# Kernel tuning notes

Measured on AMD Instinct MI355X. Metric: run time of the kernel, lower is better.

## Reference

```python
import jax, jax.numpy as jnp
import numpy as np

# Static config (matches init_kwargs / chosen shapes)
B, H, W, C, NH, WS, SS = 8, 56, 56, 1024, 32, 7, 3
N = WS * WS            # tokens per window = 49
HID = 4 * C            # mlp hidden dim
HEAD = C // NH         # 32
SCALE = HEAD ** -0.5


def _rel_pos_index():
    # Same construction as the torch buffer `relative_position_index`
    coords = np.stack(np.meshgrid(np.arange(WS), np.arange(WS), indexing='ij'))  # (2, WS, WS)
    cf = coords.reshape(2, -1)                                    # (2, N)
    rel = (cf[:, :, None] - cf[:, None, :]).transpose(1, 2, 0)    # (N, N, 2)
    rel = rel.copy()
    rel[:, :, 0] += WS - 1
    rel[:, :, 1] += WS - 1
    rel[:, :, 0] *= 2 * WS - 1
    return jnp.asarray(rel.sum(-1))                               # (N, N) int

RPI = _rel_pos_index()


def _shift_mask():
    # Standard Swin cyclic-shift attention mask (0 / -100) for Hp=H, Wp=W
    img = np.zeros((1, H, W, 1), dtype=np.float32)
    cnt = 0
    for hs in (slice(0, -WS), slice(-WS, -SS), slice(-SS, None)):
        for ws in (slice(0, -WS), slice(-WS, -SS), slice(-SS, None)):
            img[:, hs, ws, :] = cnt
            cnt += 1
    mw = img.reshape(1, H // WS, WS, W // WS, WS, 1).transpose(0, 1, 3, 2, 4, 5).reshape(-1, N)
    diff = mw[:, None, :] - mw[:, :, None]
    return jnp.asarray(np.where(diff != 0, -100.0, 0.0).astype(np.float32))  # (nW, N, N)


def _window_partition(t):
    # (B, H, W, D) -> (B*nW, N, D)
    d = t.shape[-1]
    t = t.reshape(B, H // WS, WS, W // WS, WS, d).transpose(0, 1, 3, 2, 4, 5)
    return t.reshape(-1, N, d)


def _window_reverse(w):
    # (B*nW, N, D) -> (B, H, W, D)
    d = w.shape[-1]
    w = w.reshape(B, H // WS, W // WS, WS, WS, d).transpose(0, 1, 3, 2, 4, 5)
    return w.reshape(B, H, W, d)


def _layernorm(t, g, b, eps=1e-5):
    mu = t.mean(-1, keepdims=True)
    var = ((t - mu) ** 2).mean(-1, keepdims=True)
    return (t - mu) * jax.lax.rsqrt(var + eps) * g + b


def setup_inputs() -> dict:
    key = jax.random.key(0)
    ks = jax.random.split(key, 16)
    s = 0.02
    return {
        'x': jax.random.normal(ks[0], (B, H * W, C), jnp.float32),
        'v': jax.random.normal(ks[1], (B, H, W, C), jnp.float32),
        'mask_matrix': _shift_mask(),
        'norm1_g': jnp.ones((C,), jnp.float32),
        'norm1_b': jnp.zeros((C,), jnp.float32),
        'qk_w': jax.random.normal(ks[2], (2 * C, C), jnp.float32) * s,
        'qk_b': jnp.zeros((2 * C,), jnp.float32),
        'rpb_table': jax.random.normal(ks[3], ((2 * WS - 1) ** 2, NH), jnp.float32) * s,
        'proj_w': jax.random.normal(ks[4], (C, C), jnp.float32) * s,
        'proj_b': jnp.zeros((C,), jnp.float32),
        'norm2_g': jnp.ones((C,), jnp.float32),
        'norm2_b': jnp.zeros((C,), jnp.float32),
        'fc1_w': jax.random.normal(ks[5], (HID, C), jnp.float32) * s,
        'fc1_b': jnp.zeros((HID,), jnp.float32),
        'fc2_w': jax.random.normal(ks[6], (C, HID), jnp.float32) * s,
        'fc2_b': jnp.zeros((C,), jnp.float32),
    }


def reference(x, v, mask_matrix, norm1_g, norm1_b, qk_w, qk_b, rpb_table,
              proj_w, proj_b, norm2_g, norm2_b, fc1_w, fc1_b, fc2_w, fc2_b):
    shortcut = x                                             # (B, L, C)
    xn = _layernorm(x, norm1_g, norm1_b).reshape(B, H, W, C)
    # H, W divisible by WS -> no padding. Cyclic shift (shift_size > 0).
    sx = jnp.roll(xn, (-SS, -SS), axis=(1, 2))
    sv = jnp.roll(v, (-SS, -SS), axis=(1, 2))
    xw = _window_partition(sx)                               # (B_, N, C)
    vw = _window_partition(sv)                               # (B_, N, C)
    B_ = xw.shape[0]
    # q, k projections
    qk = (xw @ qk_w.T + qk_b).reshape(B_, N, 2, NH, HEAD)
    q = qk[:, :, 0].transpose(0, 2, 1, 3) * SCALE            # (B_, h, N, d)
    k = qk[:, :, 1].transpose(0, 2, 1, 3)
    attn = jnp.einsum('bhnd,bhmd->bhnm', q, k)               # (B_, h, N, N)
    bias = rpb_table[RPI].transpose(2, 0, 1)                 # (h, N, N)
    attn = attn + bias[None]
    nW = mask_matrix.shape[0]
    attn = attn.reshape(B_ // nW, nW, NH, N, N) + mask_matrix[None, :, None]
    attn = jax.nn.softmax(attn.reshape(B_, NH, N, N), axis=-1)
    vh = vw.reshape(B_, N, NH, HEAD).transpose(0, 2, 1, 3)   # (B_, h, N, d)
    o = jnp.einsum('bhnm,bhmd->bhnd', attn, vh)
    o = o.transpose(0, 2, 1, 3).reshape(B_, N, C)
    o = o @ proj_w.T + proj_b
    # reverse windows and shift
    xr = _window_reverse(o)
    xr = jnp.roll(xr, (SS, SS), axis=(1, 2)).reshape(B, H * W, C)
    x = shortcut + xr                                        # residual (drop_path = 0)
    hdn = _layernorm(x, norm2_g, norm2_b)
    hdn = jax.nn.gelu(hdn @ fc1_w.T + fc1_b, approximate=False)
    hdn = hdn @ fc2_w.T + fc2_b
    return x + hdn
```

## Files before the change

kernel.cpp:

```cpp
#include <hip/hip_runtime.h>
#include <math.h>

typedef __attribute__((ext_vector_type(8))) short bf16x8;
typedef __attribute__((ext_vector_type(4))) short short4v;
typedef __attribute__((ext_vector_type(4))) float f32x4;

#define SCALE 0.17677669529663687f

__device__ __forceinline__ short f2bf(float f) {
  unsigned u = __builtin_bit_cast(unsigned, f);
  unsigned r = u + 0x7fffu + ((u >> 16) & 1u);
  return (short)(r >> 16);
}

__device__ __forceinline__ void gll16(const short* g, short* l) {
  __builtin_amdgcn_global_load_lds(
      (const __attribute__((address_space(1))) unsigned int*)g,
      (__attribute__((address_space(3))) unsigned int*)l, 16, 0, 0);
}

__global__ __launch_bounds__(256) void cast_qkw_kernel(const float* __restrict__ src,
                                                       short* __restrict__ dst) {
  size_t i = (size_t)blockIdx.x * 256 + threadIdx.x;
  f32x4 v = *(const f32x4*)(src + i * 4);
  float sc = (i * 4 < (size_t)1024 * 1024) ? SCALE : 1.0f;
  short4v o;
#pragma unroll
  for (int j = 0; j < 4; ++j) o[j] = f2bf(v[j] * sc);
  *(short4v*)(dst + i * 4) = o;
}

__global__ __launch_bounds__(256) void cast_kernel(const float* __restrict__ src,
                                                   short* __restrict__ dst) {
  size_t i = (size_t)blockIdx.x * 256 + threadIdx.x;
  f32x4 v = *(const f32x4*)(src + i * 4);
  short4v o;
#pragma unroll
  for (int j = 0; j < 4; ++j) o[j] = f2bf(v[j]);
  *(short4v*)(dst + i * 4) = o;
}

__global__ __launch_bounds__(256) void ln1_permute_kernel(
    const float* __restrict__ x,
    const float* __restrict__ g1, const float* __restrict__ b1,
    short* __restrict__ xnw) {
  int r = blockIdx.x;
  int b = r / 3136, rem = r % 3136;
  int wi = rem / 49, n = rem % 49;
  int hs = (wi >> 3) * 7 + n / 7, wsf = (wi & 7) * 7 + n % 7;
  int ho = hs + 3; if (ho >= 56) ho -= 56;
  int wo = wsf + 3; if (wo >= 56) wo -= 56;
  size_t src = ((size_t)b * 3136 + ho * 56 + wo) * 1024;
  int t = threadIdx.x;
  f32x4 xv = *(const f32x4*)(x + src + t * 4);
  float s = xv[0] + xv[1] + xv[2] + xv[3];
  float s2 = xv[0] * xv[0] + xv[1] * xv[1] + xv[2] * xv[2] + xv[3] * xv[3];
#pragma unroll
  for (int m = 1; m < 64; m <<= 1) { s += __shfl_xor(s, m); s2 += __shfl_xor(s2, m); }
  __shared__ float red[8];
  int w = t >> 6;
  if ((t & 63) == 0) { red[w * 2] = s; red[w * 2 + 1] = s2; }
  __syncthreads();
  float ts = red[0] + red[2] + red[4] + red[6];
  float ts2 = red[1] + red[3] + red[5] + red[7];
  float mu = ts * (1.0f / 1024.0f);
  float var = ts2 * (1.0f / 1024.0f) - mu * mu;
  float rs = rsqrtf(var + 1e-5f);
  short4v xo;
#pragma unroll
  for (int j = 0; j < 4; ++j) {
    int cc = t * 4 + j;
    xo[j] = f2bf((xv[j] - mu) * rs * g1[cc] + b1[cc]);
  }
  *(short4v*)(xnw + (size_t)r * 1024 + t * 4) = xo;
}

__global__ __launch_bounds__(256) void ln2_kernel(const float* __restrict__ x2,
                                                  const float* __restrict__ g2,
                                                  const float* __restrict__ b2,
                                                  short* __restrict__ xn2) {
  int r = blockIdx.x;
  size_t src = (size_t)r * 1024;
  int t = threadIdx.x;
  f32x4 xv = *(const f32x4*)(x2 + src + t * 4);
  float s = xv[0] + xv[1] + xv[2] + xv[3];
  float s2 = xv[0] * xv[0] + xv[1] * xv[1] + xv[2] * xv[2] + xv[3] * xv[3];
#pragma unroll
  for (int m = 1; m < 64; m <<= 1) { s += __shfl_xor(s, m); s2 += __shfl_xor(s2, m); }
  __shared__ float red[8];
  int w = t >> 6;
  if ((t & 63) == 0) { red[w * 2] = s; red[w * 2 + 1] = s2; }
  __syncthreads();
  float ts = red[0] + red[2] + red[4] + red[6];
  float ts2 = red[1] + red[3] + red[5] + red[7];
  float mu = ts * (1.0f / 1024.0f);
  float var = ts2 * (1.0f / 1024.0f) - mu * mu;
  float rs = rsqrtf(var + 1e-5f);
  short4v xo;
#pragma unroll
  for (int j = 0; j < 4; ++j) {
    int cc = t * 4 + j;
    xo[j] = f2bf((xv[j] - mu) * rs * g2[cc] + b2[cc]);
  }
  *(short4v*)(xn2 + src + t * 4) = xo;
}

template <int EPI>
__global__ __launch_bounds__(512, 2) void gemm8(const short* __restrict__ A,
                                                const short* __restrict__ Bt,
                                                const float* __restrict__ bias,
                                                const float* __restrict__ add0,
                                                void* __restrict__ out, int N, int K) {
  __shared__ __align__(16) short lds[65536];
  char* basec = (char*)lds;
  int t = threadIdx.x;
  int l = t & 63;
  int w = t >> 6;
  int wm = w >> 2, wn = w & 3;
  int g = l >> 4, c = l & 15;
  int nwg = gridDim.x * gridDim.y;
  int orig = blockIdx.y * gridDim.x + blockIdx.x;
  int q = nwg >> 3, rr = nwg & 7, xcd = orig & 7, idx = orig >> 3;
  int swz = (xcd < rr ? xcd * (q + 1) : rr * (q + 1) + (xcd - rr) * q) + idx;
  int bx = swz % gridDim.x, by = swz / gridDim.x;
  const short* Ab = A + (size_t)bx * 256 * K;
  const short* Bb = Bt + (size_t)by * 256 * K;
  int o0 = t * 16, o1 = 8192 + t * 16;
  int ol0 = o0 ^ (((o0 >> 9) & 1) << 5);
  int ol1 = o1 ^ (((o1 >> 9) & 1) << 5);
  size_t off0 = (size_t)(ol0 >> 6) * K + ((ol0 & 63) >> 1);
  size_t off1 = (size_t)(ol1 >> 6) * K + ((ol1 & 63) >> 1);
  int NT = K >> 6;
  int NI = NT >> 1;

  f32x4 acc[8][4] = {};
  bf16x8 af[8], bf2[2];

#define STAGE_A(sdb, sks, tt)                                      \
  do {                                                             \
    size_t kb = (size_t)(tt) * 64 + (sks) * 32;                    \
    short* rA = (short*)(basec + (sdb) * 65536 + (sks) * 16384);   \
    gll16(Ab + kb + off0, rA + t * 8);                             \
    gll16(Ab + kb + off1, rA + 4096 + t * 8);                      \
  } while (0)

#define STAGE_B(sdb, sks, tt)                                              \
  do {                                                                     \
    size_t kb = (size_t)(tt) * 64 + (sks) * 32;                            \
    short* rB = (short*)(basec + (sdb) * 65536 + 32768 + (sks) * 16384);   \
    gll16(Bb + kb + off0, rB + t * 8);                                     \
    gll16(Bb + kb + off1, rB + 4096 + t * 8);                              \
  } while (0)

#define DSR_A(db, ks)                                                   \
  do {                                                                  \
    _Pragma("unroll") for (int m = 0; m < 8; ++m) {                     \
      int rrow = wm * 128 + m * 16 + c;                                 \
      int lin = rrow * 64 + g * 16;                                     \
      int sw = lin ^ (((lin >> 9) & 1) << 5);                           \
      af[m] = *(const bf16x8*)(basec + (db) * 65536 + (ks) * 16384 + sw); \
    }                                                                   \
  } while (0)

#define DSR_B(db, ks, nh)                                               \
  do {                                                                  \
    _Pragma("unroll") for (int n2 = 0; n2 < 2; ++n2) {                  \
      int rB2 = wn * 64 + ((nh) * 2 + n2) * 16 + c;                     \
      int lin = rB2 * 64 + g * 16;                                      \
      int sw = lin ^ (((lin >> 9) & 1) << 5);                           \
      bf2[n2] = *(const bf16x8*)(basec + (db) * 65536 + 32768 + (ks) * 16384 + sw); \
    }                                                                   \
  } while (0)

#define SB __builtin_amdgcn_sched_barrier(0)

#define PHASE(db, ks, nh, STA, STB, sdb, sks, stt, DOW)            \
  do {                                                             \
    if ((nh) == 0) DSR_A(db, ks);                                  \
    DSR_B(db, ks, nh);                                             \
    if (STA) STAGE_A(sdb, sks, stt);                               \
    if (STB) STAGE_B(sdb, sks, stt);                               \
    if (DOW) asm volatile("s_waitcnt vmcnt(2)" ::: "memory");      \
    SB;                                                            \
    __builtin_amdgcn_s_barrier();                                  \
    SB;                                                            \
    asm volatile("s_waitcnt lgkmcnt(0)" ::: "memory");             \
    SB;                                                            \
    __builtin_amdgcn_s_setprio(1);                                 \
    _Pragma("unroll") for (int m = 0; m < 8; ++m)                  \
      _Pragma("unroll") for (int n2 = 0; n2 < 2; ++n2)             \
        acc[m][(nh) * 2 + n2] = __builtin_amdgcn_mfma_f32_16x16x32_bf16( \
            af[m], bf2[n2], acc[m][(nh) * 2 + n2], 0, 0, 0);       \
    __builtin_amdgcn_s_setprio(0);                                 \
  } while (0)

  STAGE_A(0, 0, 0);
  STAGE_B(0, 0, 0);
  STAGE_A(0, 1, 0);
  STAGE_B(0, 1, 0);
  STAGE_A(1, 0, 1);
  asm volatile("s_waitcnt vmcnt(6)" ::: "memory");
  SB;
  __builtin_amdgcn_s_barrier();
  SB;

  for (int it = 0; it < NI; ++it) {
    int t1 = 2 * it + 1;
    int nt2 = 2 * it + 2; if (nt2 > NT - 1) nt2 = NT - 1;
    int nt3 = 2 * it + 3; if (nt3 > NT - 1) nt3 = NT - 1;
    PHASE(0, 0, 0, 0, 1, 1, 0, t1, 0);
    PHASE(0, 0, 1, 1, 0, 1, 1, t1, 1);
    PHASE(0, 1, 0, 0, 1, 1, 1, t1, 0);
    PHASE(0, 1, 1, 1, 0, 0, 0, nt2, 0);
    PHASE(1, 0, 0, 0, 1, 0, 0, nt2, 0);
    PHASE(1, 0, 1, 1, 0, 0, 1, nt2, 1);
    PHASE(1, 1, 0, 0, 1, 0, 1, nt2, 0);
    PHASE(1, 1, 1, 1, 0, 1, 0, nt3, 0);
  }
  asm volatile("s_waitcnt vmcnt(0)" ::: "memory");
#undef PHASE
#undef SB
#undef DSR_B
#undef DSR_A
#undef STAGE_B
#undef STAGE_A

  int mb = bx * 256 + wm * 128;
  int nb = by * 256 + wn * 64;
#pragma unroll
  for (int m = 0; m < 8; ++m) {
#pragma unroll
    for (int i = 0; i < 4; ++i) {
      int row = mb + m * 16 + g * 4 + i;
      size_t orow = row;
      if (EPI == 1) {
        int bb = row / 3136, rem = row % 3136;
        int wi = rem / 49, n = rem % 49;
        int hs = (wi >> 3) * 7 + n / 7, wf = (wi & 7) * 7 + n % 7;
        int ho = hs + 3; if (ho >= 56) ho -= 56;
        int wo = wf + 3; if (wo >= 56) wo -= 56;
        orow = (size_t)bb * 3136 + ho * 56 + wo;
      }
#pragma unroll
      for (int nf = 0; nf < 4; ++nf) {
        int col = nb + nf * 16 + c;
        float val = acc[m][nf][i];
        if (EPI == 0) {
          float bv = bias[col] * (col < 1024 ? SCALE : 1.0f);
          ((short*)out)[(size_t)row * N + col] = f2bf(val + bv);
        } else if (EPI == 1) {
          ((float*)out)[orow * 1024 + col] = val + bias[col] + add0[orow * 1024 + col];
        } else if (EPI == 2) {
          float hv = val + bias[col];
          ((short*)out)[(size_t)row * N + col] = f2bf(0.5f * hv * (1.0f + erff(hv * 0.70710678118f)));
        } else {
          float res = add0[(size_t)row * 1024 + col];
          ((float*)out)[(size_t)row * 1024 + col] = val + bias[col] + res;
        }
      }
    }
  }
}

__global__ __launch_bounds__(256) void attn_kernel(const short* __restrict__ qk,
                                                   const float* __restrict__ v,
                                                   const float* __restrict__ rpb,
                                                   short* __restrict__ ao) {
  __shared__ __align__(16) float rpbt[32 * 169];
  __shared__ int cnt[49];
  __shared__ __align__(16) short Vt[4][32 * 72];
  __shared__ __align__(16) short Pl[4][64 * 72];
  int t = threadIdx.x, l = t & 63, w = t >> 6;
  int win = blockIdx.x >> 3;
  int h = (blockIdx.x & 7) * 4 + w;
  for (int e = t; e < 169 * 32; e += 256) {
    int hh = e / 169, idx = e - hh * 169;
    rpbt[e] = rpb[idx * 32 + hh];
  }
  if (t < 49) {
    int wi = win & 63;
    int hs = (wi >> 3) * 7 + t / 7, wsf = (wi & 7) * 7 + t % 7;
    int rh = hs < 49 ? 0 : (hs < 53 ? 1 : 2);
    int rw = wsf < 49 ? 0 : (wsf < 53 ? 1 : 2);
    cnt[t] = rh * 3 + rw;
  }
  if (l < 49) {
    int wi = win & 63, b = win >> 6;
    int hs = (wi >> 3) * 7 + l / 7, wsf = (wi & 7) * 7 + l % 7;
    int ho = hs + 3; if (ho >= 56) ho -= 56;
    int wo = wsf + 3; if (wo >= 56) wo -= 56;
    const float* vp = v + ((size_t)b * 3136 + ho * 56 + wo) * 1024 + h * 32;
#pragma unroll
    for (int d4 = 0; d4 < 8; ++d4) {
      f32x4 vv = *(const f32x4*)(vp + d4 * 4);
#pragma unroll
      for (int j = 0; j < 4; ++j) Vt[w][(d4 * 4 + j) * 72 + l] = f2bf(vv[j]);
    }
  } else {
#pragma unroll
    for (int d = 0; d < 32; ++d) Vt[w][d * 72 + l] = 0;
  }
  __syncthreads();
  int g = l >> 4, c = l & 15;
  bf16x8 qf[4], kf[4];
#pragma unroll
  for (int mt = 0; mt < 4; ++mt) {
    int r = mt * 16 + c; if (r > 48) r = 48;
    qf[mt] = *(const bf16x8*)&qk[((size_t)win * 49 + r) * 2048 + h * 32 + g * 8];
  }
#pragma unroll
  for (int nt = 0; nt < 4; ++nt) {
    int j = nt * 16 + c; if (j > 48) j = 48;
    kf[nt] = *(const bf16x8*)&qk[((size_t)win * 49 + j) * 2048 + 1024 + h * 32 + g * 8];
  }
  f32x4 s[4][4] = {};
#pragma unroll
  for (int mt = 0; mt < 4; ++mt)
#pragma unroll
    for (int nt = 0; nt < 4; ++nt)
      s[mt][nt] = __builtin_amdgcn_mfma_f32_16x16x32_bf16(qf[mt], kf[nt], s[mt][nt], 0, 0, 0);
#pragma unroll
  for (int mt = 0; mt < 4; ++mt)
#pragma unroll
    for (int nt = 0; nt < 4; ++nt)
#pragma unroll
      for (int i = 0; i < 4; ++i) {
        int r = mt * 16 + g * 4 + i;
        int j = nt * 16 + c;
        float val = s[mt][nt][i];
        if (r < 49 && j < 49) {
          int idx = (r / 7 - j / 7 + 6) * 13 + (r % 7 - j % 7 + 6);
          val += rpbt[h * 169 + idx];
          if (cnt[r] != cnt[j]) val -= 100.0f;
        } else {
          val = -1e30f;
        }
        s[mt][nt][i] = val;
      }
#pragma unroll
  for (int mt = 0; mt < 4; ++mt)
#pragma unroll
    for (int i = 0; i < 4; ++i) {
      float mx = s[mt][0][i];
#pragma unroll
      for (int nt = 1; nt < 4; ++nt) mx = fmaxf(mx, s[mt][nt][i]);
#pragma unroll
      for (int m2 = 1; m2 < 16; m2 <<= 1) mx = fmaxf(mx, __shfl_xor(mx, m2));
      float sum = 0.0f;
#pragma unroll
      for (int nt = 0; nt < 4; ++nt) {
        float e = __expf(s[mt][nt][i] - mx);
        s[mt][nt][i] = e;
        sum += e;
      }
#pragma unroll
      for (int m2 = 1; m2 < 16; m2 <<= 1) sum += __shfl_xor(sum, m2);
      float inv = 1.0f / sum;
#pragma unroll
      for (int nt = 0; nt < 4; ++nt) s[mt][nt][i] *= inv;
    }
#pragma unroll
  for (int mt = 0; mt < 4; ++mt)
#pragma unroll
    for (int nt = 0; nt < 4; ++nt)
#pragma unroll
      for (int i = 0; i < 4; ++i) {
        int r = mt * 16 + g * 4 + i, j = nt * 16 + c;
        Pl[w][r * 72 + j] = f2bf(s[mt][nt][i]);
      }
  __syncthreads();
  f32x4 o[4][2] = {};
#pragma unroll
  for (int kk = 0; kk < 2; ++kk) {
    bf16x8 vb[2];
#pragma unroll
    for (int n2 = 0; n2 < 2; ++n2)
      vb[n2] = *(const bf16x8*)&Vt[w][(n2 * 16 + c) * 72 + kk * 32 + g * 8];
#pragma unroll
    for (int mt = 0; mt < 4; ++mt) {
      bf16x8 pa = *(const bf16x8*)&Pl[w][(mt * 16 + c) * 72 + kk * 32 + g * 8];
#pragma unroll
      for (int n2 = 0; n2 < 2; ++n2)
        o[mt][n2] = __builtin_amdgcn_mfma_f32_16x16x32_bf16(pa, vb[n2], o[mt][n2], 0, 0, 0);
    }
  }
#pragma unroll
  for (int mt = 0; mt < 4; ++mt)
#pragma unroll
    for (int n2 = 0; n2 < 2; ++n2)
#pragma unroll
      for (int i = 0; i < 4; ++i) {
        int r = mt * 16 + g * 4 + i;
        if (r < 49) {
          int d = n2 * 16 + c;
          ao[((size_t)win * 49 + r) * 1024 + h * 32 + d] = f2bf(o[mt][n2][i]);
        }
      }
}

extern "C" void kernel_launch(void* const* d_in, const int* in_sizes, int n_in,
                              void* d_out, int out_size, void* d_ws, size_t ws_size,
                              hipStream_t stream) {
  (void)in_sizes; (void)n_in; (void)out_size; (void)ws_size;
  const float* x = (const float*)d_in[0];
  const float* v = (const float*)d_in[1];
  const float* n1g = (const float*)d_in[3];
  const float* n1b = (const float*)d_in[4];
  const float* qkw = (const float*)d_in[5];
  const float* qkb = (const float*)d_in[6];
  const float* rpb = (const float*)d_in[7];
  const float* pjw = (const float*)d_in[8];
  const float* pjb = (const float*)d_in[9];
  const float* n2g = (const float*)d_in[10];
  const float* n2b = (const float*)d_in[11];
  const float* f1w = (const float*)d_in[12];
  const float* f1b = (const float*)d_in[13];
  const float* f2w = (const float*)d_in[14];
  const float* f2b = (const float*)d_in[15];
  char* ws = (char*)d_ws;
  short* w_qk = (short*)(ws + 0);
  short* w_pj = (short*)(ws + 4194304);
  short* w_f1 = (short*)(ws + 6291456);
  short* w_f2 = (short*)(ws + 14680064);
  short* xnw  = (short*)(ws + 23068672);
  short* qkbuf= (short*)(ws + 74448896);
  short* aob  = (short*)(ws + 23068672);
  short* xn2  = (short*)(ws + 23068672);
  short* h1   = (short*)(ws + 74448896);
  float* out = (float*)d_out;

  cast_qkw_kernel<<<2048, 256, 0, stream>>>(qkw, w_qk);
  cast_kernel<<<1024, 256, 0, stream>>>(pjw, w_pj);
  cast_kernel<<<4096, 256, 0, stream>>>(f1w, w_f1);
  cast_kernel<<<4096, 256, 0, stream>>>(f2w, w_f2);
  ln1_permute_kernel<<<25088, 256, 0, stream>>>(x, n1g, n1b, xnw);
  gemm8<0><<<dim3(98, 8), 512, 0, stream>>>(xnw, w_qk, qkb, nullptr, qkbuf, 2048, 1024);
  attn_kernel<<<4096, 256, 0, stream>>>(qkbuf, v, rpb, aob);
  gemm8<1><<<dim3(98, 4), 512, 0, stream>>>(aob, w_pj, pjb, x, out, 1024, 1024);
  ln2_kernel<<<25088, 256, 0, stream>>>(out, n2g, n2b, xn2);
  for (int ch = 0; ch < 2; ++ch) {
    const short* a1 = xn2 + (size_t)ch * 12544 * 1024;
    float* o2 = out + (size_t)ch * 12544 * 1024;
    gemm8<2><<<dim3(49, 16), 512, 0, stream>>>(a1, w_f1, f1b, nullptr, h1, 4096, 1024);
    gemm8<3><<<dim3(49, 4), 512, 0, stream>>>(h1, w_f2, f2b, o2, o2, 1024, 4096);
  }
}
```

Measured before the change: 1.093 ms.

## Make GEMMs persistent with cross-tile prefetch and switch GELU to tanh form

Converts the tiled GEMM into a persistent kernel launched with 256 blocks (196 for fc2) that loop over output tiles. Loads for the next tile are issued while the current tile's last k-steps and epilogue run, to hide tile start-up latency and the pipeline drain. Separately, the fc1 epilogue replaces the exact erf GELU with the tanh approximation computed through expf. That is cheaper but deviates numerically from the reference exact GELU.

```diff
diff --git a/kernel.cpp b/kernel.cpp
--- a/kernel.cpp
+++ b/kernel.cpp
@@ -106,11 +106,12 @@
 }
 
 template <int EPI>
-__global__ __launch_bounds__(512, 2) void gemm8(const short* __restrict__ A,
-                                                const short* __restrict__ Bt,
-                                                const float* __restrict__ bias,
-                                                const float* __restrict__ add0,
-                                                void* __restrict__ out, int N, int K) {
+__global__ __launch_bounds__(512, 2) void gemm8p(const short* __restrict__ A,
+                                                 const short* __restrict__ Bt,
+                                                 const float* __restrict__ bias,
+                                                 const float* __restrict__ add0,
+                                                 void* __restrict__ out, int N, int K,
+                                                 int ntm, int ntot) {
   __shared__ __align__(16) short lds[65536];
   char* basec = (char*)lds;
   int t = threadIdx.x;
@@ -118,38 +119,37 @@
   int w = t >> 6;
   int wm = w >> 2, wn = w & 3;
   int g = l >> 4, c = l & 15;
-  int nwg = gridDim.x * gridDim.y;
-  int orig = blockIdx.y * gridDim.x + blockIdx.x;
-  int q = nwg >> 3, rr = nwg & 7, xcd = orig & 7, idx = orig >> 3;
-  int swz = (xcd < rr ? xcd * (q + 1) : rr * (q + 1) + (xcd - rr) * q) + idx;
-  int bx = swz % gridDim.x, by = swz / gridDim.x;
-  const short* Ab = A + (size_t)bx * 256 * K;
-  const short* Bb = Bt + (size_t)by * 256 * K;
+  int G = gridDim.x;
+  int orig = blockIdx.x;
+  int q = G >> 3, rr8 = G & 7, xcd = orig & 7, idx = orig >> 3;
+  int tau = (xcd < rr8 ? xcd * (q + 1) : rr8 * (q + 1) + (xcd - rr8) * q) + idx;
+  int bx = tau % ntm, by = tau / ntm;
+  int tauN = tau + G; if (tauN >= ntot) tauN = tau;
+  int bxN = tauN % ntm, byN = tauN / ntm;
+  const short* AbC = A + (size_t)bx * 256 * K;
+  const short* BbC = Bt + (size_t)by * 256 * K;
+  const short* AbN = A + (size_t)bxN * 256 * K;
+  const short* BbN = Bt + (size_t)byN * 256 * K;
   int o0 = t * 16, o1 = 8192 + t * 16;
   int ol0 = o0 ^ (((o0 >> 9) & 1) << 5);
   int ol1 = o1 ^ (((o1 >> 9) & 1) << 5);
   size_t off0 = (size_t)(ol0 >> 6) * K + ((ol0 & 63) >> 1);
   size_t off1 = (size_t)(ol1 >> 6) * K + ((ol1 & 63) >> 1);
   int NT = K >> 6;
-  int NI = NT >> 1;
+  int NIH = NT >> 1;
 
   f32x4 acc[8][4] = {};
   bf16x8 af[8], bf2[2];
 
-#define STAGE_A(sdb, sks, tt)                                      \
-  do {                                                             \
-    size_t kb = (size_t)(tt) * 64 + (sks) * 32;                    \
-    short* rA = (short*)(basec + (sdb) * 65536 + (sks) * 16384);   \
-    gll16(Ab + kb + off0, rA + t * 8);                             \
-    gll16(Ab + kb + off1, rA + 4096 + t * 8);                      \
-  } while (0)
-
-#define STAGE_B(sdb, sks, tt)                                              \
-  do {                                                                     \
-    size_t kb = (size_t)(tt) * 64 + (sks) * 32;                            \
-    short* rB = (short*)(basec + (sdb) * 65536 + 32768 + (sks) * 16384);   \
-    gll16(Bb + kb + off0, rB + t * 8);                                     \
-    gll16(Bb + kb + off1, rB + 4096 + t * 8);                              \
+#define STG(isA, sdb, sks, rel)                                               \
+  do {                                                                        \
+    int rl = (rel);                                                           \
+    const short* bse = (rl < NT) ? ((isA) ? AbC : BbC) : ((isA) ? AbN : BbN); \
+    int tt = rl & (NT - 1);                                                   \
+    size_t kb = (size_t)tt * 64 + (sks) * 32;                                 \
+    short* rg = (short*)(basec + (sdb) * 65536 + ((isA) ? 0 : 32768) + (sks) * 16384); \
+    gll16(bse + kb + off0, rg + t * 8);                                       \
+    gll16(bse + kb + off1, rg + 4096 + t * 8);                                \
   } while (0)
 
 #define DSR_A(db, ks)                                                   \
@@ -174,12 +174,11 @@
 
 #define SB __builtin_amdgcn_sched_barrier(0)
 
-#define PHASE(db, ks, nh, STA, STB, sdb, sks, stt, DOW)            \
+#define PHASE(db, ks, nh, isA, sdb, sks, rel, DOW)                 \
   do {                                                             \
     if ((nh) == 0) DSR_A(db, ks);                                  \
     DSR_B(db, ks, nh);                                             \
-    if (STA) STAGE_A(sdb, sks, stt);                               \
-    if (STB) STAGE_B(sdb, sks, stt);                               \
+    STG(isA, sdb, sks, rel);                                       \
     if (DOW) asm volatile("s_waitcnt vmcnt(2)" ::: "memory");      \
     SB;                                                            \
     __builtin_amdgcn_s_barrier();                                  \
@@ -194,72 +193,86 @@
     __builtin_amdgcn_s_setprio(0);                                 \
   } while (0)
 
-  STAGE_A(0, 0, 0);
-  STAGE_B(0, 0, 0);
-  STAGE_A(0, 1, 0);
-  STAGE_B(0, 1, 0);
-  STAGE_A(1, 0, 1);
+  STG(1, 0, 0, 0);
+  STG(0, 0, 0, 0);
+  STG(1, 0, 1, 0);
+  STG(0, 0, 1, 0);
+  STG(1, 1, 0, 1);
   asm volatile("s_waitcnt vmcnt(6)" ::: "memory");
   SB;
   __builtin_amdgcn_s_barrier();
   SB;
 
-  for (int it = 0; it < NI; ++it) {
-    int t1 = 2 * it + 1;
-    int nt2 = 2 * it + 2; if (nt2 > NT - 1) nt2 = NT - 1;
-    int nt3 = 2 * it + 3; if (nt3 > NT - 1) nt3 = NT - 1;
-    PHASE(0, 0, 0, 0, 1, 1, 0, t1, 0);
-    PHASE(0, 0, 1, 1, 0, 1, 1, t1, 1);
-    PHASE(0, 1, 0, 0, 1, 1, 1, t1, 0);
-    PHASE(0, 1, 1, 1, 0, 0, 0, nt2, 0);
-    PHASE(1, 0, 0, 0, 1, 0, 0, nt2, 0);
-    PHASE(1, 0, 1, 1, 0, 0, 1, nt2, 1);
-    PHASE(1, 1, 0, 0, 1, 0, 1, nt2, 0);
-    PHASE(1, 1, 1, 1, 0, 1, 0, nt3, 0);
-  }
-  asm volatile("s_waitcnt vmcnt(0)" ::: "memory");
+  while (true) {
+    for (int iti = 0; iti < NIH; ++iti) {
+      int s0 = 2 * iti;
+      PHASE(0, 0, 0, 0, 1, 0, s0 + 1, 0);
+      PHASE(0, 0, 1, 1, 1, 1, s0 + 1, 1);
+      PHASE(0, 1, 0, 0, 1, 1, s0 + 1, 0);
+      PHASE(0, 1, 1, 1, 0, 0, s0 + 2, 0);
+      PHASE(1, 0, 0, 0, 0, 0, s0 + 2, 0);
+      PHASE(1, 0, 1, 1, 0, 1, s0 + 2, 1);
+      PHASE(1, 1, 0, 0, 0, 1, s0 + 2, 0);
+      PHASE(1, 1, 1, 1, 1, 0, s0 + 3, 0);
+    }
+    {
+      int mb = bx * 256 + wm * 128;
+      int nb = by * 256 + wn * 64;
+#pragma unroll
+      for (int m = 0; m < 8; ++m) {
+#pragma unroll
+        for (int i = 0; i < 4; ++i) {
+          int row = mb + m * 16 + g * 4 + i;
+          size_t orow = row;
+          if (EPI == 1) {
+            int bb = row / 3136, rem = row % 3136;
+            int wi = rem / 49, n = rem % 49;
+            int hs = (wi >> 3) * 7 + n / 7, wf = (wi & 7) * 7 + n % 7;
+            int ho = hs + 3; if (ho >= 56) ho -= 56;
+            int wo = wf + 3; if (wo >= 56) wo -= 56;
+            orow = (size_t)bb * 3136 + ho * 56 + wo;
+          }
+#pragma unroll
+          for (int nf = 0; nf < 4; ++nf) {
+            int col = nb + nf * 16 + c;
+            float val = acc[m][nf][i];
+            if (EPI == 0) {
+              float bv = bias[col] * (col < 1024 ? SCALE : 1.0f);
+              ((short*)out)[(size_t)row * N + col] = f2bf(val + bv);
+            } else if (EPI == 1) {
+              ((float*)out)[orow * 1024 + col] = val + bias[col] + add0[orow * 1024 + col];
+            } else if (EPI == 2) {
+              float hv = val + bias[col];
+              float z2 = 1.5957691216f * hv * (1.0f + 0.044715f * hv * hv);
+              float th = 1.0f - 2.0f / (__expf(z2) + 1.0f);
+              ((short*)out)[(size_t)row * N + col] = f2bf(0.5f * hv * (1.0f + th));
+            } else {
+              float res = add0[(size_t)row * 1024 + col];
+              ((float*)out)[(size_t)row * 1024 + col] = val + bias[col] + res;
+            }
+          }
+        }
+      }
+    }
+    tau += G;
+    if (tau >= ntot) break;
+    bx = bxN; by = byN; AbC = AbN; BbC = BbN;
+    int tau2 = tau + G; if (tau2 >= ntot) tau2 = tau;
+    bxN = tau2 % ntm; byN = tau2 / ntm;
+    AbN = A + (size_t)bxN * 256 * K;
+    BbN = Bt + (size_t)byN * 256 * K;
+#pragma unroll
+    for (int m = 0; m < 8; ++m)
+#pragma unroll
+      for (int nf = 0; nf < 4; ++nf)
+#pragma unroll
+        for (int i = 0; i < 4; ++i) acc[m][nf][i] = 0.0f;
+  }
 #undef PHASE
 #undef SB
 #undef DSR_B
 #undef DSR_A
-#undef STAGE_B
-#undef STAGE_A
-
-  int mb = bx * 256 + wm * 128;
-  int nb = by * 256 + wn * 64;
-#pragma unroll
-  for (int m = 0; m < 8; ++m) {
-#pragma unroll
-    for (int i = 0; i < 4; ++i) {
-      int row = mb + m * 16 + g * 4 + i;
-      size_t orow = row;
-      if (EPI == 1) {
-        int bb = row / 3136, rem = row % 3136;
-        int wi = rem / 49, n = rem % 49;
-        int hs = (wi >> 3) * 7 + n / 7, wf = (wi & 7) * 7 + n % 7;
-        int ho = hs + 3; if (ho >= 56) ho -= 56;
-        int wo = wf + 3; if (wo >= 56) wo -= 56;
-        orow = (size_t)bb * 3136 + ho * 56 + wo;
-      }
-#pragma unroll
-      for (int nf = 0; nf < 4; ++nf) {
-        int col = nb + nf * 16 + c;
-        float val = acc[m][nf][i];
-        if (EPI == 0) {
-          float bv = bias[col] * (col < 1024 ? SCALE : 1.0f);
-          ((short*)out)[(size_t)row * N + col] = f2bf(val + bv);
-        } else if (EPI == 1) {
-          ((float*)out)[orow * 1024 + col] = val + bias[col] + add0[orow * 1024 + col];
-        } else if (EPI == 2) {
-          float hv = val + bias[col];
-          ((short*)out)[(size_t)row * N + col] = f2bf(0.5f * hv * (1.0f + erff(hv * 0.70710678118f)));
-        } else {
-          float res = add0[(size_t)row * 1024 + col];
-          ((float*)out)[(size_t)row * 1024 + col] = val + bias[col] + res;
-        }
-      }
-    }
-  }
+#undef STG
 }
 
 __global__ __launch_bounds__(256) void attn_kernel(const short* __restrict__ qk,
@@ -434,14 +447,14 @@
   cast_kernel<<<4096, 256, 0, stream>>>(f1w, w_f1);
   cast_kernel<<<4096, 256, 0, stream>>>(f2w, w_f2);
   ln1_permute_kernel<<<25088, 256, 0, stream>>>(x, n1g, n1b, xnw);
-  gemm8<0><<<dim3(98, 8), 512, 0, stream>>>(xnw, w_qk, qkb, nullptr, qkbuf, 2048, 1024);
+  gemm8p<0><<<256, 512, 0, stream>>>(xnw, w_qk, qkb, nullptr, qkbuf, 2048, 1024, 98, 784);
   attn_kernel<<<4096, 256, 0, stream>>>(qkbuf, v, rpb, aob);
-  gemm8<1><<<dim3(98, 4), 512, 0, stream>>>(aob, w_pj, pjb, x, out, 1024, 1024);
+  gemm8p<1><<<256, 512, 0, stream>>>(aob, w_pj, pjb, x, out, 1024, 1024, 98, 392);
   ln2_kernel<<<25088, 256, 0, stream>>>(out, n2g, n2b, xn2);
   for (int ch = 0; ch < 2; ++ch) {
     const short* a1 = xn2 + (size_t)ch * 12544 * 1024;
     float* o2 = out + (size_t)ch * 12544 * 1024;
-    gemm8<2><<<dim3(49, 16), 512, 0, stream>>>(a1, w_f1, f1b, nullptr, h1, 4096, 1024);
-    gemm8<3><<<dim3(49, 4), 512, 0, stream>>>(h1, w_f2, f2b, o2, o2, 1024, 4096);
-  }
-}
+    gemm8p<2><<<256, 512, 0, stream>>>(a1, w_f1, f1b, nullptr, h1, 4096, 1024, 49, 784);
+    gemm8p<3><<<196, 512, 0, stream>>>(h1, w_f2, f2b, o2, o2, 1024, 4096, 49, 196);
+  }
+}
```

After: 1.072 ms. About the same (-1.9%).
